# Kernel optimization log

Hardware: AMD Instinct MI355X
Metric: run time of the kernel (lower is better)

Reference implementation:

```python
import jax, jax.numpy as jnp
import numpy as np

N_NODES = 50000
N_EDGES = 600000
D_IN = 128
H = 128
D_OUT = 1


def setup_inputs() -> dict:
    key = jax.random.key(0)
    ks = jax.random.split(key, 6)
    x = jax.random.normal(ks[0], (N_NODES, D_IN), dtype=jnp.float32)
    edge_index = jax.random.randint(ks[1], (2, N_EDGES), 0, N_NODES, dtype=jnp.int32)
    # Glorot-ish init for GCN weights
    W1 = jax.random.normal(ks[2], (D_IN, H), dtype=jnp.float32) / np.sqrt(D_IN)
    W2 = jax.random.normal(ks[3], (H, H), dtype=jnp.float32) / np.sqrt(H)
    W3 = jax.random.normal(ks[4], (H, D_OUT), dtype=jnp.float32) / np.sqrt(H)
    b1 = jnp.zeros((H,), jnp.float32)
    b2 = jnp.zeros((H,), jnp.float32)
    b3 = jnp.zeros((D_OUT,), jnp.float32)
    return {"x": x, "edge_index": edge_index, "W1": W1, "b1": b1,
            "W2": W2, "b2": b2, "W3": W3, "b3": b3}


def _gcn_layer(h, src, dst, norm, self_norm, W, b, n_nodes):
    # GCNConv: h' = D^{-1/2}(A+I)D^{-1/2} (h W) + b
    hw = h @ W                                        # [N, F_out]
    msg = hw[src] * norm[:, None]                     # [E, F_out] edge gather
    agg = jax.ops.segment_sum(msg, dst, num_segments=n_nodes)
    agg = agg + hw * self_norm[:, None]               # self-loop contribution
    return agg + b


def reference(x, edge_index, W1, b1, W2, b2, W3, b3):
    # NOTE: F.dropout treated as identity (deterministic eval reference).
    n = x.shape[0]
    src, dst = edge_index[0], edge_index[1]
    # symmetric normalization with self-loops (PyG gcn_norm, edge_weight=1)
    deg = jnp.zeros((n,), x.dtype).at[dst].add(1.0) + 1.0
    dis = jax.lax.rsqrt(deg)                          # deg^{-1/2}
    norm = dis[src] * dis[dst]                        # per-edge norm
    self_norm = dis * dis
    h = jax.nn.relu(_gcn_layer(x, src, dst, norm, self_norm, W1, b1, n))
    h = jax.nn.relu(_gcn_layer(h, src, dst, norm, self_norm, W2, b2, n))
    h = jax.nn.relu(_gcn_layer(h, src, dst, norm, self_norm, W3, b3, n))
    return h
```

## Files before the change

kernel.cpp:

```cpp
#include <hip/hip_runtime.h>
#include <hip/hip_fp16.h>


typedef _Float16 v8h __attribute__((ext_vector_type(8)));
typedef float v4f __attribute__((ext_vector_type(4)));

__global__ __launch_bounds__(256) void k_count_wcast(const int* __restrict__ dst,
                                                     int* __restrict__ cnt,
                                                     int* __restrict__ rank, int nE,
                                                     int BE,
                                                     const float* __restrict__ W1,
                                                     const float* __restrict__ W2,
                                                     __half* __restrict__ Wt1,
                                                     __half* __restrict__ Wt2) {
    int b = blockIdx.x;
    if (b < BE) {
        int e = b * 256 + threadIdx.x;
        if (e < nE) rank[e] = atomicAdd(&cnt[dst[e]], 1);
    } else {
        int i = (b - BE) * 256 + threadIdx.x;
        int k = i >> 7, c = i & 127;
        Wt1[c * 128 + k] = __float2half(W1[i]);
        Wt2[c * 128 + k] = __float2half(W2[i]);
    }
}

__global__ __launch_bounds__(256) void k_scan_blk(const int* __restrict__ cnt,
                                                  float* __restrict__ dis,
                                                  int* __restrict__ excl,
                                                  int* __restrict__ blk_sum, int nN) {
    __shared__ int sm[256];
    const int t = threadIdx.x;
    int i = blockIdx.x * 256 + t;
    int v = (i < nN) ? cnt[i] : 0;
    if (i < nN) dis[i] = rsqrtf((float)v + 1.0f);
    sm[t] = v;
    __syncthreads();
#pragma unroll
    for (int off = 1; off < 256; off <<= 1) {
        int x = (t >= off) ? sm[t - off] : 0;
        __syncthreads();
        sm[t] += x;
        __syncthreads();
    }
    if (i < nN) excl[i] = sm[t] - v;
    if (t == 255) blk_sum[blockIdx.x] = sm[255];
}

__global__ __launch_bounds__(256) void k_scan_add(const int* __restrict__ excl,
                                                  const int* __restrict__ blk_sum,
                                                  int* __restrict__ row_ptr,
                                                  int nN, int nB) {
    __shared__ int sm[256];
    const int t = threadIdx.x;
    int v = (t < nB) ? blk_sum[t] : 0;
    sm[t] = v;
    __syncthreads();
#pragma unroll
    for (int off = 1; off < 256; off <<= 1) {
        int x = (t >= off) ? sm[t - off] : 0;
        __syncthreads();
        sm[t] += x;
        __syncthreads();
    }
    int i = blockIdx.x * 256 + t;
    if (i < nN) {
        int b = i >> 8;
        row_ptr[i] = excl[i] + sm[b] - blk_sum[b];
    }
    if (i == 0) row_ptr[nN] = sm[255];
}

__device__ __forceinline__ void add8(float acc[8], float4 r) {
    __half2* hp = (__half2*)&r;
#pragma unroll
    for (int k = 0; k < 4; ++k) {
        float2 f = __half22float2(hp[k]);
        acc[2 * k] += f.x;
        acc[2 * k + 1] += f.y;
    }
}

__device__ __forceinline__ void gather_row16(const float4* __restrict__ Hv,
                                             const int* __restrict__ row_ptr,
                                             const int* __restrict__ src_csr,
                                             int g, int f8, float acc[8]) {
    int beg = row_ptr[g], end = row_ptr[g + 1];
#pragma unroll
    for (int k = 0; k < 8; ++k) acc[k] = 0.f;
    add8(acc, Hv[(size_t)g * 16 + f8]);
    int e = beg;
    for (; e + 4 <= end; e += 4) {
        int s[4];
#pragma unroll
        for (int j = 0; j < 4; ++j) s[j] = src_csr[e + j];
        float4 r[4];
#pragma unroll
        for (int j = 0; j < 4; ++j) r[j] = Hv[(size_t)s[j] * 16 + f8];
#pragma unroll
        for (int j = 0; j < 4; ++j) add8(acc, r[j]);
    }
    for (; e < end; ++e) add8(acc, Hv[(size_t)src_csr[e] * 16 + f8]);
}

__global__ __launch_bounds__(256) void k_gemm_bin(const float* __restrict__ X32,
                                                  const __half* __restrict__ Wt,
                                                  const float* __restrict__ dis,
                                                  __half* __restrict__ HWS,
                                                  int nrows, int BG,
                                                  const int* __restrict__ src,
                                                  const int* __restrict__ dst,
                                                  const int* __restrict__ rank,
                                                  const int* __restrict__ row_ptr,
                                                  int* __restrict__ src_csr, int nE) {
    __shared__ __half xs[64 * 136];
    if (blockIdx.x >= BG) {
        int e = (blockIdx.x - BG) * 256 + threadIdx.x;
        if (e < nE) {
            int d = dst[e];
            src_csr[row_ptr[d] + rank[e]] = src[e];
        }
        return;
    }

    const int t = threadIdx.x;
    const int row0 = blockIdx.x * 64;

#pragma unroll
    for (int i = 0; i < 8; ++i) {
        int f = t + i * 256;
        int r = f >> 5, k4 = f & 31;
        int gr = row0 + r;
        float4 v = make_float4(0.f, 0.f, 0.f, 0.f);
        if (gr < nrows) v = ((const float4*)X32)[(size_t)gr * 32 + k4];
        __half2 h01 = __float22half2_rn(make_float2(v.x, v.y));
        __half2 h23 = __float22half2_rn(make_float2(v.z, v.w));
        float2 packed;
        *(__half2*)&packed.x = h01;
        *(__half2*)&packed.y = h23;
        *(float2*)&xs[r * 136 + k4 * 4] = packed;
    }
    __syncthreads();

    const int w = t >> 6;
    const int l = t & 63;
    const int mrow = l & 15;
    const int kq = l >> 4;

    v8h a[4];
#pragma unroll
    for (int kk = 0; kk < 4; ++kk)
        a[kk] = *(const v8h*)&xs[(w * 16 + mrow) * 136 + kk * 32 + kq * 8];

    v4f acc[8];
#pragma unroll
    for (int c = 0; c < 8; ++c) acc[c] = (v4f){0.f, 0.f, 0.f, 0.f};

#pragma unroll
    for (int kk = 0; kk < 4; ++kk) {
#pragma unroll
        for (int c = 0; c < 8; ++c) {
            v8h b = *(const v8h*)&Wt[(size_t)(c * 16 + mrow) * 128 + kk * 32 + kq * 8];
            acc[c] = __builtin_amdgcn_mfma_f32_16x16x32_f16(a[kk], b, acc[c], 0, 0, 0);
        }
    }

    float dn[4];
#pragma unroll
    for (int r = 0; r < 4; ++r) {
        int grow = row0 + w * 16 + kq * 4 + r;
        dn[r] = (grow < nrows) ? dis[grow] : 0.f;
    }
#pragma unroll
    for (int c = 0; c < 8; ++c) {
#pragma unroll
        for (int r = 0; r < 4; ++r) {
            int grow = row0 + w * 16 + kq * 4 + r;
            if (grow < nrows)
                HWS[(size_t)grow * 128 + c * 16 + mrow] =
                    __float2half(acc[c][r] * dn[r]);
        }
    }
}

__global__ __launch_bounds__(512) void k_gather_gemm(const __half* __restrict__ HWS1,
                                                     const int* __restrict__ row_ptr,
                                                     const int* __restrict__ src_csr,
                                                     const float* __restrict__ dis,
                                                     const float* __restrict__ bias,
                                                     const __half* __restrict__ Wt,
                                                     __half* __restrict__ HWS2,
                                                     int nN) {
    __shared__ __half xs[64 * 136];
    __shared__ int q;
    const int t = threadIdx.x;
    const int row0 = blockIdx.x * 64;
    const int l = t & 63;
    const int f8 = t & 15;
    const int qbase = l & 48;
    const float4* Hv = (const float4*)HWS1;

    float bv[8];
    *(float4*)&bv[0] = ((const float4*)bias)[f8 * 2];
    *(float4*)&bv[4] = ((const float4*)bias)[f8 * 2 + 1];

    if (t == 0) q = 0;
    __syncthreads();

    for (;;) {
        int lr = 0;
        if (f8 == 0) lr = atomicAdd(&q, 1);
        lr = __shfl(lr, qbase, 64);
        if (lr >= 64) break;
        int g = row0 + lr;
        float acc[8];
        __half2 h[4];
        if (g < nN) {
            gather_row16(Hv, row_ptr, src_csr, g, f8, acc);
            float dn = dis[g];
#pragma unroll
            for (int k = 0; k < 4; ++k)
                h[k] = __float22half2_rn(make_float2(
                    fmaxf(acc[2 * k] * dn + bv[2 * k], 0.f),
                    fmaxf(acc[2 * k + 1] * dn + bv[2 * k + 1], 0.f)));
        } else {
#pragma unroll
            for (int k = 0; k < 4; ++k) h[k] = __float2half2_rn(0.f);
        }
        *(float4*)&xs[lr * 136 + f8 * 8] = *(float4*)h;
    }
    __syncthreads();

    const int w = t >> 6;
    const int mrow = l & 15;
    const int kq = l >> 4;
    const int rgrp = (w & 3) * 16;
    const int cgrp = (w >> 2) * 4;

    v8h a[4];
#pragma unroll
    for (int kk = 0; kk < 4; ++kk)
        a[kk] = *(const v8h*)&xs[(rgrp + mrow) * 136 + kk * 32 + kq * 8];

    v4f acc[4];
#pragma unroll
    for (int c = 0; c < 4; ++c) acc[c] = (v4f){0.f, 0.f, 0.f, 0.f};

#pragma unroll
    for (int kk = 0; kk < 4; ++kk) {
#pragma unroll
        for (int c = 0; c < 4; ++c) {
            v8h b = *(const v8h*)&Wt[(size_t)((cgrp + c) * 16 + mrow) * 128 + kk * 32 + kq * 8];
            acc[c] = __builtin_amdgcn_mfma_f32_16x16x32_f16(a[kk], b, acc[c], 0, 0, 0);
        }
    }

    float dn4[4];
#pragma unroll
    for (int r = 0; r < 4; ++r) {
        int grow = row0 + rgrp + kq * 4 + r;
        dn4[r] = (grow < nN) ? dis[grow] : 0.f;
    }
#pragma unroll
    for (int c = 0; c < 4; ++c) {
#pragma unroll
        for (int r = 0; r < 4; ++r) {
            int grow = row0 + rgrp + kq * 4 + r;
            if (grow < nN)
                HWS2[(size_t)grow * 128 + (cgrp + c) * 16 + mrow] =
                    __float2half(acc[c][r] * dn4[r]);
        }
    }
}

__global__ __launch_bounds__(256) void k_gather_gemv(const __half* __restrict__ HWS2,
                                                     const int* __restrict__ row_ptr,
                                                     const int* __restrict__ src_csr,
                                                     const float* __restrict__ dis,
                                                     const float* __restrict__ bias,
                                                     const float* __restrict__ W3,
                                                     float* __restrict__ hw3s, int nN) {
    int g = blockIdx.x * 16 + (threadIdx.x >> 4);
    if (g >= nN) return;
    int f8 = threadIdx.x & 15;
    float acc[8];
    gather_row16((const float4*)HWS2, row_ptr, src_csr, g, f8, acc);
    float dn = dis[g];
    float bv[8], w3[8];
    *(float4*)&bv[0] = ((const float4*)bias)[f8 * 2];
    *(float4*)&bv[4] = ((const float4*)bias)[f8 * 2 + 1];
    *(float4*)&w3[0] = ((const float4*)W3)[f8 * 2];
    *(float4*)&w3[4] = ((const float4*)W3)[f8 * 2 + 1];
    float sum = 0.f;
#pragma unroll
    for (int k = 0; k < 8; ++k)
        sum += fmaxf(acc[k] * dn + bv[k], 0.f) * w3[k];
#pragma unroll
    for (int off = 8; off > 0; off >>= 1) sum += __shfl_down(sum, off, 16);
    if (f8 == 0) hw3s[g] = sum * dn;
}

__global__ __launch_bounds__(256) void k_gather3(const float* __restrict__ hw3s,
                                                 const int* __restrict__ row_ptr,
                                                 const int* __restrict__ src_csr,
                                                 const float* __restrict__ dis,
                                                 const float* __restrict__ b3,
                                                 float* __restrict__ out, int nN) {
    int i = blockIdx.x * 256 + threadIdx.x;
    if (i >= nN) return;
    float acc = hw3s[i];
    int beg = row_ptr[i], end = row_ptr[i + 1];
    for (int e = beg; e < end; ++e) acc += hw3s[src_csr[e]];
    out[i] = fmaxf(acc * dis[i] + b3[0], 0.f);
}

extern "C" void kernel_launch(void* const* d_in, const int* in_sizes, int n_in,
                              void* d_out, int out_size, void* d_ws, size_t ws_size,
                              hipStream_t stream) {
    const float* x  = (const float*)d_in[0];
    const int*   ei = (const int*)d_in[1];
    const float* W1 = (const float*)d_in[2];
    const float* b1 = (const float*)d_in[3];
    const float* W2 = (const float*)d_in[4];
    const float* b2 = (const float*)d_in[5];
    const float* W3 = (const float*)d_in[6];
    const float* b3 = (const float*)d_in[7];

    const int nN = in_sizes[0] / 128;
    const int nE = in_sizes[1] / 2;
    const int* src = ei;
    const int* dst = ei + nE;

    const int nB = (nN + 255) / 256;

    char* p = (char*)d_ws;
    int*    cnt      = (int*)p;           p += (size_t)nN * 4;
    int*    excl     = (int*)p;           p += (size_t)nN * 4;
    int*    blk_sum  = (int*)p;           p += (size_t)(nB + 1) * 4;
    int*    row_ptr  = (int*)p;           p += (size_t)(nN + 1) * 4;
    int*    rank     = (int*)p;           p += (size_t)nE * 4;
    int*    src_csr  = (int*)p;           p += (size_t)nE * 4;
    float*  dis      = (float*)p;         p += (size_t)nN * 4;
    float*  hw3s     = (float*)p;         p += (size_t)nN * 4;
    p = (char*)(((uintptr_t)p + 255) & ~(uintptr_t)255);
    __half* Wt1      = (__half*)p;        p += (size_t)128 * 128 * 2;
    __half* Wt2      = (__half*)p;        p += (size_t)128 * 128 * 2;
    __half* bufA     = (__half*)p;        p += (size_t)nN * 128 * 2;
    p = (char*)(((uintptr_t)p + 255) & ~(uintptr_t)255);
    __half* bufB     = (__half*)p;        p += (size_t)nN * 128 * 2;

    const int BE  = (nE + 255) / 256;
    const int BN  = (nN + 255) / 256;
    const int BG  = (nN + 63) / 64;
    const int BGV = (nN + 15) / 16;

    hipMemsetAsync(cnt, 0, (size_t)nN * sizeof(int), stream);
    k_count_wcast<<<BE + 64, 256, 0, stream>>>(dst, cnt, rank, nE, BE,
                                               W1, W2, Wt1, Wt2);
    k_scan_blk<<<nB, 256, 0, stream>>>(cnt, dis, excl, blk_sum, nN);
    k_scan_add<<<nB, 256, 0, stream>>>(excl, blk_sum, row_ptr, nN, nB);

    k_gemm_bin<<<BG + BE, 256, 0, stream>>>(x, Wt1, dis, bufA, nN, BG,
                                            src, dst, rank, row_ptr, src_csr, nE);

    k_gather_gemm<<<BG, 512, 0, stream>>>(bufA, row_ptr, src_csr, dis, b1, Wt2,
                                          bufB, nN);

    k_gather_gemv<<<BGV, 256, 0, stream>>>(bufB, row_ptr, src_csr, dis, b2, W3,
                                           hw3s, nN);

    k_gather3<<<BN, 256, 0, stream>>>(hw3s, row_ptr, src_csr, dis, b3,
                                      (float*)d_out, nN);
}
```

Baseline: 211.9 us.

## Fuse degree counting with layer-1 GEMM, defer dis scaling, sort CSR rows

The memset is replaced by a zeroing kernel that also casts the weights. The edge-degree atomic count now runs in the same launch as the layer-1 GEMM, so the GEMM no longer waits for the scan. The dis scaling of the layer-1 output moves into a separate pass fused with CSR binning, which costs one extra read and write of the fp16 feature matrix. A new warp sort orders each CSR row's source indices (rows with at most 32 edges) to improve gather locality, at the cost of one more launch.

```diff
diff --git a/kernel.cpp b/kernel.cpp
--- a/kernel.cpp
+++ b/kernel.cpp
@@ -5,126 +5,41 @@
 typedef _Float16 v8h __attribute__((ext_vector_type(8)));
 typedef float v4f __attribute__((ext_vector_type(4)));
 
-__global__ __launch_bounds__(256) void k_count_wcast(const int* __restrict__ dst,
-                                                     int* __restrict__ cnt,
-                                                     int* __restrict__ rank, int nE,
-                                                     int BE,
-                                                     const float* __restrict__ W1,
-                                                     const float* __restrict__ W2,
-                                                     __half* __restrict__ Wt1,
-                                                     __half* __restrict__ Wt2) {
+__global__ __launch_bounds__(256) void k_zero_wcast(int* __restrict__ cnt, int nN,
+                                                    int BZ,
+                                                    const float* __restrict__ W1,
+                                                    const float* __restrict__ W2,
+                                                    __half* __restrict__ Wt1,
+                                                    __half* __restrict__ Wt2) {
     int b = blockIdx.x;
-    if (b < BE) {
-        int e = b * 256 + threadIdx.x;
-        if (e < nE) rank[e] = atomicAdd(&cnt[dst[e]], 1);
+    if (b < BZ) {
+        int i = b * 256 + threadIdx.x;
+        if (i < nN) cnt[i] = 0;
     } else {
-        int i = (b - BE) * 256 + threadIdx.x;
+        int i = (b - BZ) * 256 + threadIdx.x;
         int k = i >> 7, c = i & 127;
         Wt1[c * 128 + k] = __float2half(W1[i]);
         Wt2[c * 128 + k] = __float2half(W2[i]);
     }
 }
 
-__global__ __launch_bounds__(256) void k_scan_blk(const int* __restrict__ cnt,
-                                                  float* __restrict__ dis,
-                                                  int* __restrict__ excl,
-                                                  int* __restrict__ blk_sum, int nN) {
-    __shared__ int sm[256];
+__global__ __launch_bounds__(256) void k_count_gemm(const int* __restrict__ dst,
+                                                    int* __restrict__ cnt,
+                                                    int* __restrict__ rank, int nE,
+                                                    int BE,
+                                                    const float* __restrict__ X32,
+                                                    const __half* __restrict__ Wt,
+                                                    __half* __restrict__ HWS,
+                                                    int nrows) {
+    __shared__ __half xs[64 * 136];
+    if (blockIdx.x < BE) {
+        int e = blockIdx.x * 256 + threadIdx.x;
+        if (e < nE) rank[e] = atomicAdd(&cnt[dst[e]], 1);
+        return;
+    }
+
     const int t = threadIdx.x;
-    int i = blockIdx.x * 256 + t;
-    int v = (i < nN) ? cnt[i] : 0;
-    if (i < nN) dis[i] = rsqrtf((float)v + 1.0f);
-    sm[t] = v;
-    __syncthreads();
-#pragma unroll
-    for (int off = 1; off < 256; off <<= 1) {
-        int x = (t >= off) ? sm[t - off] : 0;
-        __syncthreads();
-        sm[t] += x;
-        __syncthreads();
-    }
-    if (i < nN) excl[i] = sm[t] - v;
-    if (t == 255) blk_sum[blockIdx.x] = sm[255];
-}
-
-__global__ __launch_bounds__(256) void k_scan_add(const int* __restrict__ excl,
-                                                  const int* __restrict__ blk_sum,
-                                                  int* __restrict__ row_ptr,
-                                                  int nN, int nB) {
-    __shared__ int sm[256];
-    const int t = threadIdx.x;
-    int v = (t < nB) ? blk_sum[t] : 0;
-    sm[t] = v;
-    __syncthreads();
-#pragma unroll
-    for (int off = 1; off < 256; off <<= 1) {
-        int x = (t >= off) ? sm[t - off] : 0;
-        __syncthreads();
-        sm[t] += x;
-        __syncthreads();
-    }
-    int i = blockIdx.x * 256 + t;
-    if (i < nN) {
-        int b = i >> 8;
-        row_ptr[i] = excl[i] + sm[b] - blk_sum[b];
-    }
-    if (i == 0) row_ptr[nN] = sm[255];
-}
-
-__device__ __forceinline__ void add8(float acc[8], float4 r) {
-    __half2* hp = (__half2*)&r;
-#pragma unroll
-    for (int k = 0; k < 4; ++k) {
-        float2 f = __half22float2(hp[k]);
-        acc[2 * k] += f.x;
-        acc[2 * k + 1] += f.y;
-    }
-}
-
-__device__ __forceinline__ void gather_row16(const float4* __restrict__ Hv,
-                                             const int* __restrict__ row_ptr,
-                                             const int* __restrict__ src_csr,
-                                             int g, int f8, float acc[8]) {
-    int beg = row_ptr[g], end = row_ptr[g + 1];
-#pragma unroll
-    for (int k = 0; k < 8; ++k) acc[k] = 0.f;
-    add8(acc, Hv[(size_t)g * 16 + f8]);
-    int e = beg;
-    for (; e + 4 <= end; e += 4) {
-        int s[4];
-#pragma unroll
-        for (int j = 0; j < 4; ++j) s[j] = src_csr[e + j];
-        float4 r[4];
-#pragma unroll
-        for (int j = 0; j < 4; ++j) r[j] = Hv[(size_t)s[j] * 16 + f8];
-#pragma unroll
-        for (int j = 0; j < 4; ++j) add8(acc, r[j]);
-    }
-    for (; e < end; ++e) add8(acc, Hv[(size_t)src_csr[e] * 16 + f8]);
-}
-
-__global__ __launch_bounds__(256) void k_gemm_bin(const float* __restrict__ X32,
-                                                  const __half* __restrict__ Wt,
-                                                  const float* __restrict__ dis,
-                                                  __half* __restrict__ HWS,
-                                                  int nrows, int BG,
-                                                  const int* __restrict__ src,
-                                                  const int* __restrict__ dst,
-                                                  const int* __restrict__ rank,
-                                                  const int* __restrict__ row_ptr,
-                                                  int* __restrict__ src_csr, int nE) {
-    __shared__ __half xs[64 * 136];
-    if (blockIdx.x >= BG) {
-        int e = (blockIdx.x - BG) * 256 + threadIdx.x;
-        if (e < nE) {
-            int d = dst[e];
-            src_csr[row_ptr[d] + rank[e]] = src[e];
-        }
-        return;
-    }
-
-    const int t = threadIdx.x;
-    const int row0 = blockIdx.x * 64;
+    const int row0 = (blockIdx.x - BE) * 64;
 
 #pragma unroll
     for (int i = 0; i < 8; ++i) {
@@ -165,22 +80,146 @@
         }
     }
 
-    float dn[4];
-#pragma unroll
-    for (int r = 0; r < 4; ++r) {
-        int grow = row0 + w * 16 + kq * 4 + r;
-        dn[r] = (grow < nrows) ? dis[grow] : 0.f;
-    }
 #pragma unroll
     for (int c = 0; c < 8; ++c) {
 #pragma unroll
         for (int r = 0; r < 4; ++r) {
             int grow = row0 + w * 16 + kq * 4 + r;
             if (grow < nrows)
-                HWS[(size_t)grow * 128 + c * 16 + mrow] =
-                    __float2half(acc[c][r] * dn[r]);
-        }
-    }
+                HWS[(size_t)grow * 128 + c * 16 + mrow] = __float2half(acc[c][r]);
+        }
+    }
+}
+
+__global__ __launch_bounds__(256) void k_scan_blk(const int* __restrict__ cnt,
+                                                  float* __restrict__ dis,
+                                                  int* __restrict__ excl,
+                                                  int* __restrict__ blk_sum, int nN) {
+    __shared__ int sm[256];
+    const int t = threadIdx.x;
+    int i = blockIdx.x * 256 + t;
+    int v = (i < nN) ? cnt[i] : 0;
+    if (i < nN) dis[i] = rsqrtf((float)v + 1.0f);
+    sm[t] = v;
+    __syncthreads();
+#pragma unroll
+    for (int off = 1; off < 256; off <<= 1) {
+        int x = (t >= off) ? sm[t - off] : 0;
+        __syncthreads();
+        sm[t] += x;
+        __syncthreads();
+    }
+    if (i < nN) excl[i] = sm[t] - v;
+    if (t == 255) blk_sum[blockIdx.x] = sm[255];
+}
+
+__global__ __launch_bounds__(256) void k_scan_add(const int* __restrict__ excl,
+                                                  const int* __restrict__ blk_sum,
+                                                  int* __restrict__ row_ptr,
+                                                  int nN, int nB) {
+    __shared__ int sm[256];
+    const int t = threadIdx.x;
+    int v = (t < nB) ? blk_sum[t] : 0;
+    sm[t] = v;
+    __syncthreads();
+#pragma unroll
+    for (int off = 1; off < 256; off <<= 1) {
+        int x = (t >= off) ? sm[t - off] : 0;
+        __syncthreads();
+        sm[t] += x;
+        __syncthreads();
+    }
+    int i = blockIdx.x * 256 + t;
+    if (i < nN) {
+        int b = i >> 8;
+        row_ptr[i] = excl[i] + sm[b] - blk_sum[b];
+    }
+    if (i == 0) row_ptr[nN] = sm[255];
+}
+
+__global__ __launch_bounds__(256) void k_bin_scale(const int* __restrict__ src,
+                                                   const int* __restrict__ dst,
+                                                   const int* __restrict__ rank,
+                                                   const int* __restrict__ row_ptr,
+                                                   int* __restrict__ src_csr, int nE,
+                                                   int BE,
+                                                   const float* __restrict__ dis,
+                                                   __half* __restrict__ HWS, int nN) {
+    int b = blockIdx.x;
+    if (b < BE) {
+        int e = b * 256 + threadIdx.x;
+        if (e < nE) {
+            int d = dst[e];
+            src_csr[row_ptr[d] + rank[e]] = src[e];
+        }
+        return;
+    }
+    int i = (b - BE) * 256 + threadIdx.x;
+    if (i < nN * 16) {
+        int g = i >> 4;
+        float dn = dis[g];
+        float4 v = ((const float4*)HWS)[i];
+        __half2* hp = (__half2*)&v;
+#pragma unroll
+        for (int k = 0; k < 4; ++k) {
+            float2 f = __half22float2(hp[k]);
+            hp[k] = __float22half2_rn(make_float2(f.x * dn, f.y * dn));
+        }
+        ((float4*)HWS)[i] = v;
+    }
+}
+
+__global__ __launch_bounds__(256) void k_sortrows(const int* __restrict__ row_ptr,
+                                                  int* __restrict__ src_csr, int nN) {
+    int r = blockIdx.x * 8 + (threadIdx.x >> 5);
+    if (r >= nN) return;
+    const int l = threadIdx.x & 31;
+    int beg = row_ptr[r], end = row_ptr[r + 1];
+    int n = end - beg;
+    if (n <= 1 || n > 32) return;
+    int v = (l < n) ? src_csr[beg + l] : 0x7fffffff;
+#pragma unroll
+    for (int p = 0; p < 32; ++p) {
+        bool up = ((l + p) & 1) == 0;
+        int partner = up ? l + 1 : l - 1;
+        if (partner < 0) partner = 0;
+        if (partner > 31) partner = 31;
+        int o = __shfl(v, partner, 32);
+        if (partner != l) v = up ? min(v, o) : max(v, o);
+    }
+    if (l < n) src_csr[beg + l] = v;
+}
+
+__device__ __forceinline__ void add8(float acc[8], float4 r) {
+    __half2* hp = (__half2*)&r;
+#pragma unroll
+    for (int k = 0; k < 4; ++k) {
+        float2 f = __half22float2(hp[k]);
+        acc[2 * k] += f.x;
+        acc[2 * k + 1] += f.y;
+    }
+}
+
+__device__ __forceinline__ void gather_row16(const float4* __restrict__ Hv,
+                                             const int* __restrict__ row_ptr,
+                                             const int* __restrict__ src_csr,
+                                             int g, int f8, float acc[8]) {
+    int beg = row_ptr[g], end = row_ptr[g + 1];
+#pragma unroll
+    for (int k = 0; k < 8; ++k) acc[k] = 0.f;
+    add8(acc, Hv[(size_t)g * 16 + f8]);
+    int e = beg;
+    for (; e + 4 <= end; e += 4) {
+        int s[4];
+#pragma unroll
+        for (int j = 0; j < 4; ++j) s[j] = src_csr[e + j];
+        float4 r[4];
+#pragma unroll
+        for (int j = 0; j < 4; ++j) r[j] = Hv[(size_t)s[j] * 16 + f8];
+#pragma unroll
+        for (int j = 0; j < 4; ++j) add8(acc, r[j]);
+    }
+    for (; e < end; ++e) add8(acc, Hv[(size_t)src_csr[e] * 16 + f8]);
 }
 
 __global__ __launch_bounds__(512) void k_gather_gemm(const __half* __restrict__ HWS1,
@@ -353,15 +392,21 @@
     const int BN  = (nN + 255) / 256;
     const int BG  = (nN + 63) / 64;
     const int BGV = (nN + 15) / 16;
-
-    hipMemsetAsync(cnt, 0, (size_t)nN * sizeof(int), stream);
-    k_count_wcast<<<BE + 64, 256, 0, stream>>>(dst, cnt, rank, nE, BE,
-                                               W1, W2, Wt1, Wt2);
+    const int BSC = (nN * 16 + 255) / 256;
+    const int BSR = (nN + 7) / 8;
+
+    k_zero_wcast<<<BN + 64, 256, 0, stream>>>(cnt, nN, BN, W1, W2, Wt1, Wt2);
+
+    k_count_gemm<<<BE + BG, 256, 0, stream>>>(dst, cnt, rank, nE, BE,
+                                              x, Wt1, bufA, nN);
+
     k_scan_blk<<<nB, 256, 0, stream>>>(cnt, dis, excl, blk_sum, nN);
     k_scan_add<<<nB, 256, 0, stream>>>(excl, blk_sum, row_ptr, nN, nB);
 
-    k_gemm_bin<<<BG + BE, 256, 0, stream>>>(x, Wt1, dis, bufA, nN, BG,
-                                            src, dst, rank, row_ptr, src_csr, nE);
+    k_bin_scale<<<BE + BSC, 256, 0, stream>>>(src, dst, rank, row_ptr, src_csr,
+                                              nE, BE, dis, bufA, nN);
+
+    k_sortrows<<<BSR, 256, 0, stream>>>(row_ptr, src_csr, nN);
 
     k_gather_gemm<<<BG, 512, 0, stream>>>(bufA, row_ptr, src_csr, dis, b1, Wt2,
                                           bufB, nN);
```

New measurement: 226.3 us. 6.8% more time.

## Overlap degree counting with first GEMM using 8-way banked counters

Applied to the files above, without the earlier changes.

Splits the degree counter into 8 banks indexed by block, which spreads atomic contention, and fuses the counting pass with the layer-1 GEMM. The GEMM no longer scales rows by dis, since dis is not yet known when it runs. The layer-2 gather now multiplies each neighbour row by dis[src], which adds a per-edge load. Binning into CSR moves to its own kernel using per-bank base offsets, and the memset is replaced by a zeroing kernel fused with the weight cast. The trade is more kernel launches and extra counter and base8 traffic.

```diff
diff --git a/kernel.cpp b/kernel.cpp
--- a/kernel.cpp
+++ b/kernel.cpp
@@ -5,126 +5,44 @@
 typedef _Float16 v8h __attribute__((ext_vector_type(8)));
 typedef float v4f __attribute__((ext_vector_type(4)));
 
-__global__ __launch_bounds__(256) void k_count_wcast(const int* __restrict__ dst,
-                                                     int* __restrict__ cnt,
-                                                     int* __restrict__ rank, int nE,
-                                                     int BE,
-                                                     const float* __restrict__ W1,
-                                                     const float* __restrict__ W2,
-                                                     __half* __restrict__ Wt1,
-                                                     __half* __restrict__ Wt2) {
+__global__ __launch_bounds__(256) void k_zero_wcast(int* __restrict__ cnt8, int n8,
+                                                    int BZ,
+                                                    const float* __restrict__ W1,
+                                                    const float* __restrict__ W2,
+                                                    __half* __restrict__ Wt1,
+                                                    __half* __restrict__ Wt2) {
     int b = blockIdx.x;
-    if (b < BE) {
-        int e = b * 256 + threadIdx.x;
-        if (e < nE) rank[e] = atomicAdd(&cnt[dst[e]], 1);
+    if (b < BZ) {
+        int i = b * 256 + threadIdx.x;
+        if (i < n8) cnt8[i] = 0;
     } else {
-        int i = (b - BE) * 256 + threadIdx.x;
+        int i = (b - BZ) * 256 + threadIdx.x;
         int k = i >> 7, c = i & 127;
         Wt1[c * 128 + k] = __float2half(W1[i]);
         Wt2[c * 128 + k] = __float2half(W2[i]);
     }
 }
 
-__global__ __launch_bounds__(256) void k_scan_blk(const int* __restrict__ cnt,
-                                                  float* __restrict__ dis,
-                                                  int* __restrict__ excl,
-                                                  int* __restrict__ blk_sum, int nN) {
-    __shared__ int sm[256];
+__global__ __launch_bounds__(256) void k_count_gemm(const int* __restrict__ dst,
+                                                    int* __restrict__ cnt8,
+                                                    int* __restrict__ rank, int nE,
+                                                    int BE, int nN,
+                                                    const float* __restrict__ X32,
+                                                    const __half* __restrict__ Wt,
+                                                    __half* __restrict__ HWS,
+                                                    int nrows) {
+    __shared__ __half xs[64 * 136];
+    if (blockIdx.x < BE) {
+        int e = blockIdx.x * 256 + threadIdx.x;
+        if (e < nE) {
+            int bank = blockIdx.x & 7;
+            rank[e] = atomicAdd(&cnt8[bank * nN + dst[e]], 1);
+        }
+        return;
+    }
+
     const int t = threadIdx.x;
-    int i = blockIdx.x * 256 + t;
-    int v = (i < nN) ? cnt[i] : 0;
-    if (i < nN) dis[i] = rsqrtf((float)v + 1.0f);
-    sm[t] = v;
-    __syncthreads();
-#pragma unroll
-    for (int off = 1; off < 256; off <<= 1) {
-        int x = (t >= off) ? sm[t - off] : 0;
-        __syncthreads();
-        sm[t] += x;
-        __syncthreads();
-    }
-    if (i < nN) excl[i] = sm[t] - v;
-    if (t == 255) blk_sum[blockIdx.x] = sm[255];
-}
-
-__global__ __launch_bounds__(256) void k_scan_add(const int* __restrict__ excl,
-                                                  const int* __restrict__ blk_sum,
-                                                  int* __restrict__ row_ptr,
-                                                  int nN, int nB) {
-    __shared__ int sm[256];
-    const int t = threadIdx.x;
-    int v = (t < nB) ? blk_sum[t] : 0;
-    sm[t] = v;
-    __syncthreads();
-#pragma unroll
-    for (int off = 1; off < 256; off <<= 1) {
-        int x = (t >= off) ? sm[t - off] : 0;
-        __syncthreads();
-        sm[t] += x;
-        __syncthreads();
-    }
-    int i = blockIdx.x * 256 + t;
-    if (i < nN) {
-        int b = i >> 8;
-        row_ptr[i] = excl[i] + sm[b] - blk_sum[b];
-    }
-    if (i == 0) row_ptr[nN] = sm[255];
-}
-
-__device__ __forceinline__ void add8(float acc[8], float4 r) {
-    __half2* hp = (__half2*)&r;
-#pragma unroll
-    for (int k = 0; k < 4; ++k) {
-        float2 f = __half22float2(hp[k]);
-        acc[2 * k] += f.x;
-        acc[2 * k + 1] += f.y;
-    }
-}
-
-__device__ __forceinline__ void gather_row16(const float4* __restrict__ Hv,
-                                             const int* __restrict__ row_ptr,
-                                             const int* __restrict__ src_csr,
-                                             int g, int f8, float acc[8]) {
-    int beg = row_ptr[g], end = row_ptr[g + 1];
-#pragma unroll
-    for (int k = 0; k < 8; ++k) acc[k] = 0.f;
-    add8(acc, Hv[(size_t)g * 16 + f8]);
-    int e = beg;
-    for (; e + 4 <= end; e += 4) {
-        int s[4];
-#pragma unroll
-        for (int j = 0; j < 4; ++j) s[j] = src_csr[e + j];
-        float4 r[4];
-#pragma unroll
-        for (int j = 0; j < 4; ++j) r[j] = Hv[(size_t)s[j] * 16 + f8];
-#pragma unroll
-        for (int j = 0; j < 4; ++j) add8(acc, r[j]);
-    }
-    for (; e < end; ++e) add8(acc, Hv[(size_t)src_csr[e] * 16 + f8]);
-}
-
-__global__ __launch_bounds__(256) void k_gemm_bin(const float* __restrict__ X32,
-                                                  const __half* __restrict__ Wt,
-                                                  const float* __restrict__ dis,
-                                                  __half* __restrict__ HWS,
-                                                  int nrows, int BG,
-                                                  const int* __restrict__ src,
-                                                  const int* __restrict__ dst,
-                                                  const int* __restrict__ rank,
-                                                  const int* __restrict__ row_ptr,
-                                                  int* __restrict__ src_csr, int nE) {
-    __shared__ __half xs[64 * 136];
-    if (blockIdx.x >= BG) {
-        int e = (blockIdx.x - BG) * 256 + threadIdx.x;
-        if (e < nE) {
-            int d = dst[e];
-            src_csr[row_ptr[d] + rank[e]] = src[e];
-        }
-        return;
-    }
-
-    const int t = threadIdx.x;
-    const int row0 = blockIdx.x * 64;
+    const int row0 = (blockIdx.x - BE) * 64;
 
 #pragma unroll
     for (int i = 0; i < 8; ++i) {
@@ -165,21 +83,158 @@
         }
     }
 
-    float dn[4];
-#pragma unroll
-    for (int r = 0; r < 4; ++r) {
-        int grow = row0 + w * 16 + kq * 4 + r;
-        dn[r] = (grow < nrows) ? dis[grow] : 0.f;
-    }
 #pragma unroll
     for (int c = 0; c < 8; ++c) {
 #pragma unroll
         for (int r = 0; r < 4; ++r) {
             int grow = row0 + w * 16 + kq * 4 + r;
             if (grow < nrows)
-                HWS[(size_t)grow * 128 + c * 16 + mrow] =
-                    __float2half(acc[c][r] * dn[r]);
-        }
+                HWS[(size_t)grow * 128 + c * 16 + mrow] = __float2half(acc[c][r]);
+        }
+    }
+}
+
+__global__ __launch_bounds__(256) void k_scan_blk(const int* __restrict__ cnt8,
+                                                  float* __restrict__ dis,
+                                                  int* __restrict__ excl,
+                                                  int* __restrict__ blk_sum, int nN) {
+    __shared__ int sm[256];
+    const int t = threadIdx.x;
+    int i = blockIdx.x * 256 + t;
+    int v = 0;
+    if (i < nN) {
+#pragma unroll
+        for (int b = 0; b < 8; ++b) v += cnt8[b * nN + i];
+        dis[i] = rsqrtf((float)v + 1.0f);
+    }
+    sm[t] = v;
+    __syncthreads();
+#pragma unroll
+    for (int off = 1; off < 256; off <<= 1) {
+        int x = (t >= off) ? sm[t - off] : 0;
+        __syncthreads();
+        sm[t] += x;
+        __syncthreads();
+    }
+    if (i < nN) excl[i] = sm[t] - v;
+    if (t == 255) blk_sum[blockIdx.x] = sm[255];
+}
+
+__global__ __launch_bounds__(256) void k_scan_add(const int* __restrict__ excl,
+                                                  const int* __restrict__ blk_sum,
+                                                  const int* __restrict__ cnt8,
+                                                  int* __restrict__ row_ptr,
+                                                  int* __restrict__ base8,
+                                                  int nN, int nB) {
+    __shared__ int sm[256];
+    const int t = threadIdx.x;
+    int v = (t < nB) ? blk_sum[t] : 0;
+    sm[t] = v;
+    __syncthreads();
+#pragma unroll
+    for (int off = 1; off < 256; off <<= 1) {
+        int x = (t >= off) ? sm[t - off] : 0;
+        __syncthreads();
+        sm[t] += x;
+        __syncthreads();
+    }
+    int i = blockIdx.x * 256 + t;
+    if (i < nN) {
+        int b = i >> 8;
+        int rp = excl[i] + sm[b] - blk_sum[b];
+        row_ptr[i] = rp;
+        int off = rp;
+#pragma unroll
+        for (int bk = 0; bk < 8; ++bk) {
+            base8[i * 8 + bk] = off;
+            off += cnt8[bk * nN + i];
+        }
+    }
+    if (i == 0) row_ptr[nN] = sm[255];
+}
+
+__global__ __launch_bounds__(256) void k_bin(const int* __restrict__ src,
+                                             const int* __restrict__ dst,
+                                             const int* __restrict__ rank,
+                                             const int* __restrict__ base8,
+                                             int* __restrict__ src_csr, int nE) {
+    int e = blockIdx.x * 256 + threadIdx.x;
+    if (e < nE) {
+        int d = dst[e];
+        int bank = blockIdx.x & 7;
+        src_csr[base8[d * 8 + bank] + rank[e]] = src[e];
+    }
+}
+
+__device__ __forceinline__ void add8(float acc[8], float4 r) {
+    __half2* hp = (__half2*)&r;
+#pragma unroll
+    for (int k = 0; k < 4; ++k) {
+        float2 f = __half22float2(hp[k]);
+        acc[2 * k] += f.x;
+        acc[2 * k + 1] += f.y;
+    }
+}
+
+__device__ __forceinline__ void add8w(float acc[8], float4 r, float w) {
+    __half2* hp = (__half2*)&r;
+#pragma unroll
+    for (int k = 0; k < 4; ++k) {
+        float2 f = __half22float2(hp[k]);
+        acc[2 * k] = fmaf(f.x, w, acc[2 * k]);
+        acc[2 * k + 1] = fmaf(f.y, w, acc[2 * k + 1]);
+    }
+}
+
+__device__ __forceinline__ void gather_row16(const float4* __restrict__ Hv,
+                                             const int* __restrict__ row_ptr,
+                                             const int* __restrict__ src_csr,
+                                             int g, int f8, float acc[8]) {
+    int beg = row_ptr[g], end = row_ptr[g + 1];
+#pragma unroll
+    for (int k = 0; k < 8; ++k) acc[k] = 0.f;
+    add8(acc, Hv[(size_t)g * 16 + f8]);
+    int e = beg;
+    for (; e + 4 <= end; e += 4) {
+        int s[4];
+#pragma unroll
+        for (int j = 0; j < 4; ++j) s[j] = src_csr[e + j];
+        float4 r[4];
+#pragma unroll
+        for (int j = 0; j < 4; ++j) r[j] = Hv[(size_t)s[j] * 16 + f8];
+#pragma unroll
+        for (int j = 0; j < 4; ++j) add8(acc, r[j]);
+    }
+    for (; e < end; ++e) add8(acc, Hv[(size_t)src_csr[e] * 16 + f8]);
+}
+
+__device__ __forceinline__ void gather_row16w(const float4* __restrict__ Hv,
+                                              const int* __restrict__ row_ptr,
+                                              const int* __restrict__ src_csr,
+                                              const float* __restrict__ dis,
+                                              int g, float dg, int f8,
+                                              float acc[8]) {
+    int beg = row_ptr[g], end = row_ptr[g + 1];
+#pragma unroll
+    for (int k = 0; k < 8; ++k) acc[k] = 0.f;
+    add8w(acc, Hv[(size_t)g * 16 + f8], dg);
+    int e = beg;
+    for (; e + 4 <= end; e += 4) {
+        int s[4];
+#pragma unroll
+        for (int j = 0; j < 4; ++j) s[j] = src_csr[e + j];
+        float wv[4];
+#pragma unroll
+        for (int j = 0; j < 4; ++j) wv[j] = dis[s[j]];
+        float4 r[4];
+#pragma unroll
+        for (int j = 0; j < 4; ++j) r[j] = Hv[(size_t)s[j] * 16 + f8];
+#pragma unroll
+        for (int j = 0; j < 4; ++j) add8w(acc, r[j], wv[j]);
+    }
+    for (; e < end; ++e) {
+        int s = src_csr[e];
+        add8w(acc, Hv[(size_t)s * 16 + f8], dis[s]);
     }
 }
 
@@ -216,8 +271,8 @@
         float acc[8];
         __half2 h[4];
         if (g < nN) {
-            gather_row16(Hv, row_ptr, src_csr, g, f8, acc);
             float dn = dis[g];
+            gather_row16w(Hv, row_ptr, src_csr, dis, g, dn, f8, acc);
 #pragma unroll
             for (int k = 0; k < 4; ++k)
                 h[k] = __float22half2_rn(make_float2(
@@ -334,7 +389,8 @@
     const int nB = (nN + 255) / 256;
 
     char* p = (char*)d_ws;
-    int*    cnt      = (int*)p;           p += (size_t)nN * 4;
+    int*    cnt8     = (int*)p;           p += (size_t)nN * 8 * 4;
+    int*    base8    = (int*)p;           p += (size_t)nN * 8 * 4;
     int*    excl     = (int*)p;           p += (size_t)nN * 4;
     int*    blk_sum  = (int*)p;           p += (size_t)(nB + 1) * 4;
     int*    row_ptr  = (int*)p;           p += (size_t)(nN + 1) * 4;
@@ -353,15 +409,17 @@
     const int BN  = (nN + 255) / 256;
     const int BG  = (nN + 63) / 64;
     const int BGV = (nN + 15) / 16;
-
-    hipMemsetAsync(cnt, 0, (size_t)nN * sizeof(int), stream);
-    k_count_wcast<<<BE + 64, 256, 0, stream>>>(dst, cnt, rank, nE, BE,
-                                               W1, W2, Wt1, Wt2);
-    k_scan_blk<<<nB, 256, 0, stream>>>(cnt, dis, excl, blk_sum, nN);
-    k_scan_add<<<nB, 256, 0, stream>>>(excl, blk_sum, row_ptr, nN, nB);
-
-    k_gemm_bin<<<BG + BE, 256, 0, stream>>>(x, Wt1, dis, bufA, nN, BG,
-                                            src, dst, rank, row_ptr, src_csr, nE);
+    const int BZ8 = (nN * 8 + 255) / 256;
+
+    k_zero_wcast<<<BZ8 + 64, 256, 0, stream>>>(cnt8, nN * 8, BZ8, W1, W2, Wt1, Wt2);
+
+    k_count_gemm<<<BE + BG, 256, 0, stream>>>(dst, cnt8, rank, nE, BE, nN,
+                                              x, Wt1, bufA, nN);
+
+    k_scan_blk<<<nB, 256, 0, stream>>>(cnt8, dis, excl, blk_sum, nN);
+    k_scan_add<<<nB, 256, 0, stream>>>(excl, blk_sum, cnt8, row_ptr, base8, nN, nB);
+
+    k_bin<<<BE, 256, 0, stream>>>(src, dst, rank, base8, src_csr, nE);
 
     k_gather_gemm<<<BG, 512, 0, stream>>>(bufA, row_ptr, src_csr, dis, b1, Wt2,
                                           bufB, nN);
```

Result: slower. 222.6 us (+5.0%).
